# Performance work log

Hardware: AMD Instinct MI355X
Metric: run time of the kernel (lower is better)

Reference implementation:

```python
import jax, jax.numpy as jnp
import numpy as np

B, T, K = 8, 2048, 4          # lattices, nodes per lattice, incoming edges per node
E = T * K                     # edges per lattice
D = 256                       # input_dim
H = 256                       # hidden_dim (== input_dim, required by node_h assignment)


def setup_inputs() -> dict:
    key = jax.random.key(0)
    k1, k2, k3, k4, k5 = jax.random.split(key, 5)
    edge_input = jax.random.normal(k1, (B, E, D), dtype=jnp.float32)
    weight_ih = jax.random.normal(k2, (D, 4 * H), dtype=jnp.float32) * (1.0 / np.sqrt(D))
    weight_hh = jax.random.normal(k3, (H, 4 * H), dtype=jnp.float32) * (1.0 / np.sqrt(H))
    bias = jax.random.normal(k4, (4 * H,), dtype=jnp.float32) * 0.02
    prev_idx = jax.random.randint(k5, (T, K), 0, E, dtype=jnp.int32)  # prevs[step]
    return {"edge_input": edge_input, "weight_ih": weight_ih,
            "weight_hh": weight_hh, "bias": bias, "prev_idx": prev_idx}


def reference(edge_input, weight_ih, weight_hh, bias, prev_idx):
    # Faithful to the source: node_h/node_c read by EdgeCell at step t are row t,
    # which is only written at the END of iteration t -> always zeros when read.
    # Therefore node_hh = 0 @ weight_hh + bias = bias, and c0 = 0, and every
    # edge's gates depend only on its own input. (weight_hh thus has no effect,
    # exactly as in the original numerics.)
    pre = jnp.einsum('bed,dh->beh', edge_input, weight_ih) + bias  # [B,E,4H]
    i, f, g, o = jnp.split(pre, 4, axis=-1)
    # c = sigmoid(f)*c0 + sigmoid(i)*tanh(g), with c0 == 0
    edge_c = jax.nn.sigmoid(i) * jnp.tanh(g)                       # [B,E,H]
    # source bug kept verbatim: h = o.sigmoid() * o.tanh()
    edge_h = jax.nn.sigmoid(o) * jnp.tanh(o)                       # [B,E,H]
    # node state = mean over incoming (prev) edges
    node_h = edge_h[:, prev_idx, :].mean(axis=2)                   # [B,T,H]
    node_c = edge_c[:, prev_idx, :].mean(axis=2)                   # [B,T,H]
    return node_h, node_c, edge_h, edge_c
```

## Files before the change

kernel.cpp:

```cpp
#include <hip/hip_runtime.h>
#include <hip/hip_bf16.h>
#include <stdint.h>

typedef __attribute__((ext_vector_type(8))) __bf16 bf16x8;
typedef __attribute__((ext_vector_type(4))) float f32x4;
typedef __attribute__((ext_vector_type(4))) uint32_t u32x4;

#define B_SZ 8
#define E_SZ 8192
#define T_SZ 2048
#define D_SZ 256
#define H_SZ 256
#define NP   768

#define BM 128
#define BN 192
#define BK 64
#define NTHR 512
#define NWG  2048

#define NODE_H_OFF 0
#define NODE_C_OFF (B_SZ*T_SZ*H_SZ)
#define EDGE_H_OFF (2*B_SZ*T_SZ*H_SZ)
#define EDGE_C_OFF (2*B_SZ*T_SZ*H_SZ + B_SZ*E_SZ*H_SZ)

__device__ __forceinline__ uint32_t pk_bf16(float a, float b) {
    uint32_t ua = __float_as_uint(a);
    uint32_t ub = __float_as_uint(b);
    ua += 0x7fffu + ((ua >> 16) & 1u);
    ub += 0x7fffu + ((ub >> 16) & 1u);
    return (ua >> 16) | (ub & 0xffff0000u);
}

__global__ void wcvt_kernel(const float* __restrict__ W, const float* __restrict__ bias,
                            uint16_t* __restrict__ Wt, float* __restrict__ biasp) {
    int id = blockIdx.x * 256 + threadIdx.x;
    if (id < 256 * 768) {
        int k = id / 768;
        int q = id - k * 768;
        int col = (q < 256) ? q : (q + 256);
        int s = q >> 8;
        int j = q & 255;
        int np = 48 * (j >> 4) + 16 * s + (j & 15);
        uint32_t ua = __float_as_uint(W[k * 1024 + col]);
        ua += 0x7fffu + ((ua >> 16) & 1u);
        Wt[np * 256 + k] = (uint16_t)(ua >> 16);
        if (k == 0) biasp[np] = bias[col];
    }
}

__launch_bounds__(NTHR, 4)
__global__ void gemm_act_kernel(const float* __restrict__ A,
                                const uint16_t* __restrict__ Wt,
                                const float* __restrict__ biasp,
                                float* __restrict__ out) {
    __shared__ __align__(16) char smem[(BM + BN) * BK * 2];
    char* As = smem;
    char* Bs = smem + BM * BK * 2;

    const int tid  = threadIdx.x;
    const int bid  = blockIdx.x;
    const int wg   = (bid & 7) * (NWG / 8) + (bid >> 3);
    const int mb   = wg >> 2;
    const int nb   = wg & 3;
    const int m0   = mb * BM;
    const int n0   = nb * BN;

    const int wid  = tid >> 6;
    const int lane = tid & 63;
    const int wm   = wid >> 2;
    const int wn   = wid & 3;
    const int l15  = lane & 15;
    const int lq   = lane >> 4;

    f32x4 acc[4][3];
    #pragma unroll
    for (int mf = 0; mf < 4; ++mf)
        #pragma unroll
        for (int nf = 0; nf < 3; ++nf)
            acc[mf][nf] = (f32x4){0.f, 0.f, 0.f, 0.f};

    for (int kt = 0; kt < 4; ++kt) {
        const int k0 = kt * BK;
        #pragma unroll
        for (int r2 = 0; r2 < 3; ++r2) {
            int p   = (r2 * NTHR + tid) * 16;
            int row = p >> 7;
            int csw = (p & 127) ^ ((row & 7) << 4);
            const uint16_t* g = Wt + (n0 + row) * 256 + k0 + (csw >> 1);
            __builtin_amdgcn_global_load_lds(
                (const __attribute__((address_space(1))) uint32_t*)g,
                (__attribute__((address_space(3))) uint32_t*)(Bs + p), 16, 0, 0);
        }
        #pragma unroll
        for (int r2 = 0; r2 < 2; ++r2) {
            int id  = r2 * NTHR + tid;
            int row = id >> 3;
            int c16 = id & 7;
            const float* ga = A + (size_t)(m0 + row) * D_SZ + k0 + c16 * 8;
            f32x4 x0 = *(const f32x4*)ga;
            f32x4 x1 = *(const f32x4*)(ga + 4);
            u32x4 v = { pk_bf16(x0.x, x0.y), pk_bf16(x0.z, x0.w),
                        pk_bf16(x1.x, x1.y), pk_bf16(x1.z, x1.w) };
            int csw = (c16 * 16) ^ ((row & 7) << 4);
            *(u32x4*)(As + row * 128 + csw) = v;
        }
        __syncthreads();
        #pragma unroll
        for (int kk = 0; kk < 2; ++kk) {
            const int kb = kk * 64 + lq * 16;
            bf16x8 af[4], bfr[3];
            #pragma unroll
            for (int mf = 0; mf < 4; ++mf) {
                int row = wm * 64 + mf * 16 + l15;
                af[mf] = *(const bf16x8*)(As + row * 128 + (kb ^ ((row & 7) << 4)));
            }
            #pragma unroll
            for (int nf = 0; nf < 3; ++nf) {
                int row = wn * 48 + nf * 16 + l15;
                bfr[nf] = *(const bf16x8*)(Bs + row * 128 + (kb ^ ((row & 7) << 4)));
            }
            #pragma unroll
            for (int mf = 0; mf < 4; ++mf)
                #pragma unroll
                for (int nf = 0; nf < 3; ++nf)
                    acc[mf][nf] = __builtin_amdgcn_mfma_f32_16x16x32_bf16(
                        af[mf], bfr[nf], acc[mf][nf], 0, 0, 0);
        }
        __syncthreads();
    }

    const float L2E = 1.44269504088896340736f;
    const int jj = (nb * 4 + wn) * 16 + l15;
    const int bb = n0 + wn * 48 + l15;
    const float bi = biasp[bb];
    const float bg = biasp[bb + 16];
    const float bo = biasp[bb + 32];
    float* __restrict__ eh = out + EDGE_H_OFF;
    float* __restrict__ ec = out + EDGE_C_OFF;
    #pragma unroll
    for (int mf = 0; mf < 4; ++mf) {
        const int mbase = m0 + wm * 64 + mf * 16 + lq * 4;
        #pragma unroll
        for (int r = 0; r < 4; ++r) {
            const size_t m = (size_t)(mbase + r);
            float pi = acc[mf][0][r] + bi;
            float pg = acc[mf][1][r] + bg;
            float po = acc[mf][2][r] + bo;
            float ei = __builtin_amdgcn_exp2f(-L2E * pi);
            float eg = __builtin_amdgcn_exp2f(-2.f * L2E * pg);
            float eo = __builtin_amdgcn_exp2f(-L2E * po);
            float c  = (1.f - eg) * __builtin_amdgcn_rcpf((1.f + ei) * (1.f + eg));
            float h  = (1.f - eo) * __builtin_amdgcn_rcpf(1.f + eo * eo);
            eh[m * H_SZ + jj] = h;
            ec[m * H_SZ + jj] = c;
        }
    }
}

__global__ void node_mean_kernel(const int* __restrict__ prev,
                                 const float* __restrict__ outr,
                                 float* __restrict__ out) {
    int gid  = blockIdx.x * 4 + (threadIdx.x >> 6);
    int lane = threadIdx.x & 63;
    int b = gid >> 11;
    int t = gid & 2047;
    const float* eh = outr + EDGE_H_OFF + (size_t)b * E_SZ * H_SZ;
    const float* ec = outr + EDGE_C_OFF + (size_t)b * E_SZ * H_SZ;
    f32x4 hs = (f32x4){0.f,0.f,0.f,0.f};
    f32x4 cs = (f32x4){0.f,0.f,0.f,0.f};
    #pragma unroll
    for (int k = 0; k < 4; ++k) {
        int e = prev[t * 4 + k];
        hs += *(const f32x4*)(eh + (size_t)e * H_SZ + lane * 4);
        cs += *(const f32x4*)(ec + (size_t)e * H_SZ + lane * 4);
    }
    hs *= 0.25f; cs *= 0.25f;
    size_t o = (size_t)(b * T_SZ + t) * H_SZ + lane * 4;
    *(f32x4*)(out + NODE_H_OFF + o) = hs;
    *(f32x4*)(out + NODE_C_OFF + o) = cs;
}

extern "C" void kernel_launch(void* const* d_in, const int* in_sizes, int n_in,
                              void* d_out, int out_size, void* d_ws, size_t ws_size,
                              hipStream_t stream) {
    const float* edge_input = (const float*)d_in[0];
    const float* weight_ih  = (const float*)d_in[1];
    const float* bias       = (const float*)d_in[3];
    const int*   prev_idx   = (const int*)d_in[4];
    float* out = (float*)d_out;

    uint16_t* Wt    = (uint16_t*)d_ws;
    float*    biasp = (float*)((char*)d_ws + NP * 256 * 2);

    wcvt_kernel<<<(256 * 768 + 255) / 256, 256, 0, stream>>>(weight_ih, bias, Wt, biasp);
    gemm_act_kernel<<<NWG, NTHR, 0, stream>>>(edge_input, Wt, biasp, out);
    node_mean_kernel<<<(B_SZ * T_SZ) / 4, 256, 0, stream>>>(prev_idx, out, out);
}
```

Before: 79.90 us.

## Double-buffer LDS tiles to overlap next K-tile loads with MFMA compute

Doubles the shared memory to two A/B tile buffers. The loads for the next K tile (A through registers, B through global_load_lds) are issued before the MFMA work on the current tile, and the bf16-packed A values are stored afterwards. This aims to hide global load latency behind matrix math and cuts one barrier per iteration. In exchange, LDS use doubles to 80KB per block and register pressure rises, which can lower occupancy below the 4-blocks launch bound.

New measurement: 77.85 us. 2.6% less time.

```diff
diff --git a/kernel.cpp b/kernel.cpp
--- a/kernel.cpp
+++ b/kernel.cpp
@@ -18,6 +18,7 @@
 #define BK 64
 #define NTHR 512
 #define NWG  2048
+#define TILE_BYTES ((BM + BN) * BK * 2)
 
 #define NODE_H_OFF 0
 #define NODE_C_OFF (B_SZ*T_SZ*H_SZ)
@@ -54,9 +55,7 @@
                                 const uint16_t* __restrict__ Wt,
                                 const float* __restrict__ biasp,
                                 float* __restrict__ out) {
-    __shared__ __align__(16) char smem[(BM + BN) * BK * 2];
-    char* As = smem;
-    char* Bs = smem + BM * BK * 2;
+    __shared__ __align__(16) char smem[2 * TILE_BYTES];
 
     const int tid  = threadIdx.x;
     const int bid  = blockIdx.x;
@@ -73,6 +72,13 @@
     const int l15  = lane & 15;
     const int lq   = lane >> 4;
 
+    const int aid0  = tid;
+    const int aid1  = NTHR + tid;
+    const int arow0 = aid0 >> 3, ac0 = (aid0 & 7) * 16;
+    const int arow1 = aid1 >> 3, ac1 = (aid1 & 7) * 16;
+    const int asw0  = ac0 ^ ((arow0 & 7) << 4);
+    const int asw1  = ac1 ^ ((arow1 & 7) << 4);
+
     f32x4 acc[4][3];
     #pragma unroll
     for (int mf = 0; mf < 4; ++mf)
@@ -80,32 +86,56 @@
         for (int nf = 0; nf < 3; ++nf)
             acc[mf][nf] = (f32x4){0.f, 0.f, 0.f, 0.f};
 
-    for (int kt = 0; kt < 4; ++kt) {
-        const int k0 = kt * BK;
+    {
+        char* As = smem;
+        char* Bs = smem + BM * BK * 2;
+        const float* ga0 = A + (size_t)(m0 + arow0) * D_SZ + (ac0 >> 1);
+        const float* ga1 = A + (size_t)(m0 + arow1) * D_SZ + (ac1 >> 1);
+        f32x4 x0 = *(const f32x4*)ga0, x1 = *(const f32x4*)(ga0 + 4);
+        f32x4 x2 = *(const f32x4*)ga1, x3 = *(const f32x4*)(ga1 + 4);
         #pragma unroll
         for (int r2 = 0; r2 < 3; ++r2) {
             int p   = (r2 * NTHR + tid) * 16;
             int row = p >> 7;
             int csw = (p & 127) ^ ((row & 7) << 4);
-            const uint16_t* g = Wt + (n0 + row) * 256 + k0 + (csw >> 1);
+            const uint16_t* g = Wt + (n0 + row) * 256 + (csw >> 1);
             __builtin_amdgcn_global_load_lds(
                 (const __attribute__((address_space(1))) uint32_t*)g,
                 (__attribute__((address_space(3))) uint32_t*)(Bs + p), 16, 0, 0);
         }
-        #pragma unroll
-        for (int r2 = 0; r2 < 2; ++r2) {
-            int id  = r2 * NTHR + tid;
-            int row = id >> 3;
-            int c16 = id & 7;
-            const float* ga = A + (size_t)(m0 + row) * D_SZ + k0 + c16 * 8;
-            f32x4 x0 = *(const f32x4*)ga;
-            f32x4 x1 = *(const f32x4*)(ga + 4);
-            u32x4 v = { pk_bf16(x0.x, x0.y), pk_bf16(x0.z, x0.w),
-                        pk_bf16(x1.x, x1.y), pk_bf16(x1.z, x1.w) };
-            int csw = (c16 * 16) ^ ((row & 7) << 4);
-            *(u32x4*)(As + row * 128 + csw) = v;
-        }
-        __syncthreads();
+        u32x4 v0 = { pk_bf16(x0.x,x0.y), pk_bf16(x0.z,x0.w), pk_bf16(x1.x,x1.y), pk_bf16(x1.z,x1.w) };
+        u32x4 v1 = { pk_bf16(x2.x,x2.y), pk_bf16(x2.z,x2.w), pk_bf16(x3.x,x3.y), pk_bf16(x3.z,x3.w) };
+        *(u32x4*)(As + arow0 * 128 + asw0) = v0;
+        *(u32x4*)(As + arow1 * 128 + asw1) = v1;
+    }
+    __syncthreads();
+
+    #pragma unroll
+    for (int kt = 0; kt < 4; ++kt) {
+        char* AsC = smem + (kt & 1) * TILE_BYTES;
+        char* BsC = AsC + BM * BK * 2;
+        char* AsN = smem + ((kt + 1) & 1) * TILE_BYTES;
+        char* BsN = AsN + BM * BK * 2;
+
+        f32x4 x0, x1, x2, x3;
+        if (kt < 3) {
+            const int k0n = (kt + 1) * BK;
+            const float* ga0 = A + (size_t)(m0 + arow0) * D_SZ + k0n + (ac0 >> 1);
+            const float* ga1 = A + (size_t)(m0 + arow1) * D_SZ + k0n + (ac1 >> 1);
+            x0 = *(const f32x4*)ga0; x1 = *(const f32x4*)(ga0 + 4);
+            x2 = *(const f32x4*)ga1; x3 = *(const f32x4*)(ga1 + 4);
+            #pragma unroll
+            for (int r2 = 0; r2 < 3; ++r2) {
+                int p   = (r2 * NTHR + tid) * 16;
+                int row = p >> 7;
+                int csw = (p & 127) ^ ((row & 7) << 4);
+                const uint16_t* g = Wt + (n0 + row) * 256 + k0n + (csw >> 1);
+                __builtin_amdgcn_global_load_lds(
+                    (const __attribute__((address_space(1))) uint32_t*)g,
+                    (__attribute__((address_space(3))) uint32_t*)(BsN + p), 16, 0, 0);
+            }
+        }
+
         #pragma unroll
         for (int kk = 0; kk < 2; ++kk) {
             const int kb = kk * 64 + lq * 16;
@@ -113,12 +143,12 @@
             #pragma unroll
             for (int mf = 0; mf < 4; ++mf) {
                 int row = wm * 64 + mf * 16 + l15;
-                af[mf] = *(const bf16x8*)(As + row * 128 + (kb ^ ((row & 7) << 4)));
+                af[mf] = *(const bf16x8*)(AsC + row * 128 + (kb ^ ((row & 7) << 4)));
             }
             #pragma unroll
             for (int nf = 0; nf < 3; ++nf) {
                 int row = wn * 48 + nf * 16 + l15;
-                bfr[nf] = *(const bf16x8*)(Bs + row * 128 + (kb ^ ((row & 7) << 4)));
+                bfr[nf] = *(const bf16x8*)(BsC + row * 128 + (kb ^ ((row & 7) << 4)));
             }
             #pragma unroll
             for (int mf = 0; mf < 4; ++mf)
@@ -127,7 +157,14 @@
                     acc[mf][nf] = __builtin_amdgcn_mfma_f32_16x16x32_bf16(
                         af[mf], bfr[nf], acc[mf][nf], 0, 0, 0);
         }
-        __syncthreads();
+
+        if (kt < 3) {
+            u32x4 v0 = { pk_bf16(x0.x,x0.y), pk_bf16(x0.z,x0.w), pk_bf16(x1.x,x1.y), pk_bf16(x1.z,x1.w) };
+            u32x4 v1 = { pk_bf16(x2.x,x2.y), pk_bf16(x2.z,x2.w), pk_bf16(x3.x,x3.y), pk_bf16(x3.z,x3.w) };
+            *(u32x4*)(AsN + arow0 * 128 + asw0) = v0;
+            *(u32x4*)(AsN + arow1 * 128 + asw1) = v1;
+            __syncthreads();
+        }
     }
 
     const float L2E = 1.44269504088896340736f;
```

## Keep full-K weight tile in LDS and feed A directly from registers

Applied to the files above, without the earlier changes.

The GEMM now loads the whole K=256 weight slice for a 96-column tile into LDS once. It then streams A rows straight from global memory into MFMA operand registers with a one-step prefetch, which removes the A staging in LDS and the per-k-tile barriers. The tile becomes 128x96 with 4096 workgroups and 8 waves arranged 4x2. The trade-off is that A is re-read from global for each of 8 column tiles instead of 4, and the larger B buffer in LDS may lower occupancy. The node mean kernel also loads its four prev indices with a single vector load.

Result: slower. 160.3 us (+100.6%).

```diff
diff --git a/kernel.cpp b/kernel.cpp
--- a/kernel.cpp
+++ b/kernel.cpp
@@ -4,6 +4,7 @@
 
 typedef __attribute__((ext_vector_type(8))) __bf16 bf16x8;
 typedef __attribute__((ext_vector_type(4))) float f32x4;
+typedef __attribute__((ext_vector_type(4))) int   i32x4;
 typedef __attribute__((ext_vector_type(4))) uint32_t u32x4;
 
 #define B_SZ 8
@@ -14,10 +15,10 @@
 #define NP   768
 
 #define BM 128
-#define BN 192
-#define BK 64
+#define BN 96
 #define NTHR 512
-#define NWG  2048
+#define NWG  4096
+#define BLDS (BN * D_SZ * 2)
 
 #define NODE_H_OFF 0
 #define NODE_C_OFF (B_SZ*T_SZ*H_SZ)
@@ -54,84 +55,97 @@
                                 const uint16_t* __restrict__ Wt,
                                 const float* __restrict__ biasp,
                                 float* __restrict__ out) {
-    __shared__ __align__(16) char smem[(BM + BN) * BK * 2];
-    char* As = smem;
-    char* Bs = smem + BM * BK * 2;
+    __shared__ __align__(16) char Bs[BLDS];
 
     const int tid  = threadIdx.x;
     const int bid  = blockIdx.x;
     const int wg   = (bid & 7) * (NWG / 8) + (bid >> 3);
-    const int mb   = wg >> 2;
-    const int nb   = wg & 3;
+    const int mb   = wg >> 3;
+    const int nb   = wg & 7;
     const int m0   = mb * BM;
     const int n0   = nb * BN;
 
     const int wid  = tid >> 6;
     const int lane = tid & 63;
-    const int wm   = wid >> 2;
-    const int wn   = wid & 3;
+    const int wm   = wid >> 1;
+    const int wn   = wid & 1;
     const int l15  = lane & 15;
     const int lq   = lane >> 4;
 
-    f32x4 acc[4][3];
-    #pragma unroll
-    for (int mf = 0; mf < 4; ++mf)
+    #pragma unroll
+    for (int r2 = 0; r2 < 6; ++r2) {
+        int p    = (r2 * NTHR + tid) * 16;
+        int row  = p >> 9;
+        int cphy = p & 511;
+        int clog = cphy ^ ((row & 7) << 4);
+        const uint16_t* g = Wt + (n0 + row) * 256 + (clog >> 1);
+        __builtin_amdgcn_global_load_lds(
+            (const __attribute__((address_space(1))) uint32_t*)g,
+            (__attribute__((address_space(3))) uint32_t*)(Bs + p), 16, 0, 0);
+    }
+
+    const float* a0base = A + (size_t)(m0 + wm * 32 + l15) * D_SZ + lq * 8;
+    const float* a1base = a0base + 16 * D_SZ;
+
+    f32x4 xc[2][2];
+    xc[0][0] = *(const f32x4*)(a0base);
+    xc[0][1] = *(const f32x4*)(a0base + 4);
+    xc[1][0] = *(const f32x4*)(a1base);
+    xc[1][1] = *(const f32x4*)(a1base + 4);
+
+    __syncthreads();
+
+    f32x4 acc[2][3];
+    #pragma unroll
+    for (int mf = 0; mf < 2; ++mf)
         #pragma unroll
         for (int nf = 0; nf < 3; ++nf)
             acc[mf][nf] = (f32x4){0.f, 0.f, 0.f, 0.f};
 
-    for (int kt = 0; kt < 4; ++kt) {
-        const int k0 = kt * BK;
-        #pragma unroll
-        for (int r2 = 0; r2 < 3; ++r2) {
-            int p   = (r2 * NTHR + tid) * 16;
-            int row = p >> 7;
-            int csw = (p & 127) ^ ((row & 7) << 4);
-            const uint16_t* g = Wt + (n0 + row) * 256 + k0 + (csw >> 1);
-            __builtin_amdgcn_global_load_lds(
-                (const __attribute__((address_space(1))) uint32_t*)g,
-                (__attribute__((address_space(3))) uint32_t*)(Bs + p), 16, 0, 0);
-        }
-        #pragma unroll
-        for (int r2 = 0; r2 < 2; ++r2) {
-            int id  = r2 * NTHR + tid;
-            int row = id >> 3;
-            int c16 = id & 7;
-            const float* ga = A + (size_t)(m0 + row) * D_SZ + k0 + c16 * 8;
-            f32x4 x0 = *(const f32x4*)ga;
-            f32x4 x1 = *(const f32x4*)(ga + 4);
-            u32x4 v = { pk_bf16(x0.x, x0.y), pk_bf16(x0.z, x0.w),
-                        pk_bf16(x1.x, x1.y), pk_bf16(x1.z, x1.w) };
-            int csw = (c16 * 16) ^ ((row & 7) << 4);
-            *(u32x4*)(As + row * 128 + csw) = v;
-        }
-        __syncthreads();
-        #pragma unroll
-        for (int kk = 0; kk < 2; ++kk) {
-            const int kb = kk * 64 + lq * 16;
-            bf16x8 af[4], bfr[3];
+    const int brow0 = wn * 48 + l15;
+    #pragma unroll
+    for (int kk = 0; kk < 8; ++kk) {
+        f32x4 xn[2][2];
+        if (kk < 7) {
+            const float* ga0 = a0base + (kk + 1) * 32;
+            const float* ga1 = a1base + (kk + 1) * 32;
+            xn[0][0] = *(const f32x4*)(ga0);
+            xn[0][1] = *(const f32x4*)(ga0 + 4);
+            xn[1][0] = *(const f32x4*)(ga1);
+            xn[1][1] = *(const f32x4*)(ga1 + 4);
+        }
+        const int kb = kk * 64 + lq * 16;
+        bf16x8 bfr[3];
+        #pragma unroll
+        for (int nf = 0; nf < 3; ++nf) {
+            int row = brow0 + nf * 16;
+            bfr[nf] = *(const bf16x8*)(Bs + row * 512 + (kb ^ ((row & 7) << 4)));
+        }
+        bf16x8 af[2];
+        #pragma unroll
+        for (int mf = 0; mf < 2; ++mf) {
+            u32x4 v = { pk_bf16(xc[mf][0].x, xc[mf][0].y), pk_bf16(xc[mf][0].z, xc[mf][0].w),
+                        pk_bf16(xc[mf][1].x, xc[mf][1].y), pk_bf16(xc[mf][1].z, xc[mf][1].w) };
+            af[mf] = __builtin_bit_cast(bf16x8, v);
+        }
+        #pragma unroll
+        for (int mf = 0; mf < 2; ++mf)
             #pragma unroll
-            for (int mf = 0; mf < 4; ++mf) {
-                int row = wm * 64 + mf * 16 + l15;
-                af[mf] = *(const bf16x8*)(As + row * 128 + (kb ^ ((row & 7) << 4)));
+            for (int nf = 0; nf < 3; ++nf)
+                acc[mf][nf] = __builtin_amdgcn_mfma_f32_16x16x32_bf16(
+                    af[mf], bfr[nf], acc[mf][nf], 0, 0, 0);
+        if (kk < 7) {
+            #pragma unroll
+            for (int mf = 0; mf < 2; ++mf) {
+                xc[mf][0] = xn[mf][0];
+                xc[mf][1] = xn[mf][1];
             }
-            #pragma unroll
-            for (int nf = 0; nf < 3; ++nf) {
-                int row = wn * 48 + nf * 16 + l15;
-                bfr[nf] = *(const bf16x8*)(Bs + row * 128 + (kb ^ ((row & 7) << 4)));
-            }
-            #pragma unroll
-            for (int mf = 0; mf < 4; ++mf)
-                #pragma unroll
-                for (int nf = 0; nf < 3; ++nf)
-                    acc[mf][nf] = __builtin_amdgcn_mfma_f32_16x16x32_bf16(
-                        af[mf], bfr[nf], acc[mf][nf], 0, 0, 0);
-        }
-        __syncthreads();
+        }
     }
 
     const float L2E = 1.44269504088896340736f;
-    const int jj = (nb * 4 + wn) * 16 + l15;
+    const int jg = nb * 2 + wn;
+    const int jj = jg * 16 + l15;
     const int bb = n0 + wn * 48 + l15;
     const float bi = biasp[bb];
     const float bg = biasp[bb + 16];
@@ -139,8 +153,8 @@
     float* __restrict__ eh = out + EDGE_H_OFF;
     float* __restrict__ ec = out + EDGE_C_OFF;
     #pragma unroll
-    for (int mf = 0; mf < 4; ++mf) {
-        const int mbase = m0 + wm * 64 + mf * 16 + lq * 4;
+    for (int mf = 0; mf < 2; ++mf) {
+        const int mbase = m0 + wm * 32 + mf * 16 + lq * 4;
         #pragma unroll
         for (int r = 0; r < 4; ++r) {
             const size_t m = (size_t)(mbase + r);
@@ -167,13 +181,14 @@
     int t = gid & 2047;
     const float* eh = outr + EDGE_H_OFF + (size_t)b * E_SZ * H_SZ;
     const float* ec = outr + EDGE_C_OFF + (size_t)b * E_SZ * H_SZ;
+    i32x4 e4 = *(const i32x4*)(prev + t * 4);
     f32x4 hs = (f32x4){0.f,0.f,0.f,0.f};
     f32x4 cs = (f32x4){0.f,0.f,0.f,0.f};
     #pragma unroll
     for (int k = 0; k < 4; ++k) {
-        int e = prev[t * 4 + k];
-        hs += *(const f32x4*)(eh + (size_t)e * H_SZ + lane * 4);
-        cs += *(const f32x4*)(ec + (size_t)e * H_SZ + lane * 4);
+        size_t off = (size_t)e4[k] * H_SZ + lane * 4;
+        hs += *(const f32x4*)(eh + off);
+        cs += *(const f32x4*)(ec + off);
     }
     hs *= 0.25f; cs *= 0.25f;
     size_t o = (size_t)(b * T_SZ + t) * H_SZ + lane * 4;
```
